# Performance work log

Hardware: AMD Instinct MI355X
Metric: run time of the kernel (lower is better)

Reference implementation:

```python
import jax, jax.numpy as jnp
import numpy as np

B, N, D_FEAT = 16, 1024, 64
NPOINT, RADIUS, NSAMPLE = 512, 0.2, 32
EPS = 1e-5


def _square_distance(src, dst):
    # src [b,S,3], dst [b,N,3] -> [b,S,N]
    d = -2.0 * jnp.einsum('bsc,bnc->bsn', src, dst)
    d = d + jnp.sum(src * src, -1)[:, :, None]
    d = d + jnp.sum(dst * dst, -1)[:, None, :]
    return d


def _fps(xyz, npoint):
    # xyz [b,N,3] -> indices [b,npoint]; seeded by point farthest from the mean
    b, n, _ = xyz.shape
    centroid = jnp.mean(xyz, axis=1, keepdims=True)
    distance = jnp.minimum(jnp.full((b, n), 1e10, xyz.dtype),
                           jnp.sum((xyz - centroid) ** 2, -1))
    farthest = jnp.argmax(distance, -1)
    bidx = jnp.arange(b)

    def body(carry, _):
        dist, far = carry
        c = xyz[bidx[:, None], far[:, None]]  # [b,1,3]
        dist = jnp.minimum(dist, jnp.sum((xyz - c) ** 2, -1))
        return (dist, jnp.argmax(dist, -1)), far

    _, idx = jax.lax.scan(body, (distance, farthest), None, length=npoint)
    return idx.T  # [b, npoint]


def _gather(points, idx):
    # points [b,N,C], idx [b,...] -> [b,...,C]
    return jax.vmap(lambda p, i: p[i])(points, idx)


def _query_ball(radius, nsample, xyz, new_xyz):
    # faithful to torch: mask out-of-radius with N, full sort, take first nsample,
    # replace sentinels by the first (closest-index) in-ball point
    b, n, _ = xyz.shape
    sqr = _square_distance(new_xyz, xyz)  # [b,S,N]
    idx = jnp.where(sqr > radius ** 2, n, jnp.arange(n)[None, None, :])
    idx = jnp.sort(idx, axis=-1)[:, :, :nsample]
    first = idx[:, :, :1]
    return jnp.where(idx == n, first, idx)


def _qbn(x):
    # QBN_RM training mode: divide by per-channel RMS of detached activations
    mean = jnp.mean(jax.lax.stop_gradient(x) ** 2, axis=(0, 2, 3))
    return x / jnp.sqrt(mean + EPS)[None, :, None, None]


def _qrelu(x):
    # scale each 3-vector by mod / max(mod, 1), coefficient detached
    b3, c, s, k = x.shape
    b = b3 // 3
    xd = jax.lax.stop_gradient(x).reshape(b, 3, c, s, k)
    mod = jnp.sqrt(jnp.sum(xd * xd, axis=1))  # [b,c,s,k]
    coeff = mod / jnp.maximum(mod, 1.0)
    return jnp.broadcast_to(coeff[:, None], (b, 3, c, s, k)).reshape(b3, c, s, k) * x


def _qmaxpool(x):
    # our_mpool1d with kernel (1, nsample): pick the max-modulus sample over K,
    # gather the same index for all 3 quaternion components
    b3, c, s, k = x.shape
    b = b3 // 3
    x5 = x.reshape(b, 3, c, s, k)
    mod = jnp.sum(jax.lax.stop_gradient(x5) ** 2, axis=1)  # argmax of mod == argmax of mod^2
    idx = jnp.argmax(mod, axis=-1)  # [b,c,s]
    idxb = jnp.broadcast_to(idx[:, None, :, :, None], (b, 3, c, s, 1))
    y = jnp.take_along_axis(x5, idxb, axis=-1)[..., 0]  # [b,3,c,s]
    return y.reshape(b3, c, s)


def setup_inputs() -> dict:
    key = jax.random.key(0)
    k1, k2, k3, k4, k5 = jax.random.split(key, 5)
    xyz = jax.random.normal(k1, (B, 3, N), dtype=jnp.float32)
    points = jax.random.normal(k2, (B * 3, D_FEAT, N), dtype=jnp.float32)
    W0 = jax.random.normal(k3, (64, 66), dtype=jnp.float32) * np.sqrt(2.0 / 66)
    W1 = jax.random.normal(k4, (64, 64), dtype=jnp.float32) * np.sqrt(2.0 / 64)
    W2 = jax.random.normal(k5, (128, 64), dtype=jnp.float32) * np.sqrt(2.0 / 64)
    return {"xyz": xyz, "points": points, "W0": W0, "W1": W1, "W2": W2}


def reference(xyz, points, W0, W1, W2):
    xyz_t = xyz.transpose(0, 2, 1)      # [B,N,3]
    pts_t = points.transpose(0, 2, 1)   # [B*3,N,D]

    fps_idx = _fps(xyz_t, NPOINT)                       # [B,S]
    new_xyz = _gather(xyz_t, fps_idx)                   # [B,S,3]
    idx = _query_ball(RADIUS, NSAMPLE, xyz_t, new_xyz)  # [B,S,K]

    g_xyz = _gather(xyz_t, idx)                         # [B,S,K,3]
    g_norm = g_xyz - new_xyz[:, :, None, :]
    gx = g_xyz.transpose(0, 3, 1, 2).reshape(B * 3, NPOINT, NSAMPLE, 1)
    gn = g_norm.transpose(0, 3, 1, 2).reshape(B * 3, NPOINT, NSAMPLE, 1)
    idx3 = jnp.broadcast_to(idx[:, None], (B, 3, NPOINT, NSAMPLE)).reshape(B * 3, NPOINT, NSAMPLE)
    gp = _gather(pts_t, idx3)                           # [B*3,S,K,D]

    x = jnp.concatenate([gn, gx, gp], axis=-1)          # [B*3,S,K,D+2]
    x = x.transpose(0, 3, 1, 2)                         # [B*3,D+2,S,K]
    for W in (W0, W1, W2):
        x = jnp.einsum('bcsk,oc->bosk', x, W)           # 1x1 conv, no bias
        x = _qrelu(_qbn(x))
    new_feat = _qmaxpool(x)                             # [B*3,128,S]
    return new_xyz.transpose(0, 2, 1), new_feat
```

## Files before the change

kernel.cpp:

```cpp
#include <hip/hip_runtime.h>

typedef unsigned int u32;
typedef unsigned long long u64;
typedef float v2f __attribute__((ext_vector_type(2)));

#define NB 16
#define NPT 1024
#define NP 512
#define NS 32
#define DF 64
#define RAD2 0.04f
#define EPSQ 1e-5f
#define CNTF 786432.0f
#define NGRP 8192
#define TCAP 96
#define TSLOT 128
#define NTILE_MAX 2731
#define NBALLBLK 4096
#define NFILLBLK 1366

__device__ __forceinline__ float rmul(float a, float b){ return __fmul_rn(a,b); }
__device__ __forceinline__ float radd(float a, float b){ return __fadd_rn(a,b); }
__device__ __forceinline__ float sq3(float a, float b, float c){
  return radd(radd(rmul(a,a), rmul(b,b)), rmul(c,c));
}

__device__ __forceinline__ float wave_sum64(float v){
  #pragma unroll
  for(int m=1;m<64;m<<=1) v += __shfl_xor(v, m, 64);
  return v;
}
__device__ __forceinline__ float half_sum32(float v){
  #pragma unroll
  for(int m=1;m<32;m<<=1) v += __shfl_xor(v, m, 64);
  return v;
}

#define DPPK(CTRL) do{ \
  unsigned _lo = (unsigned)k, _hi = (unsigned)(k>>32); \
  unsigned _mlo = (unsigned)__builtin_amdgcn_mov_dpp((int)_lo, (CTRL), 0xF, 0xF, true); \
  unsigned _mhi = (unsigned)__builtin_amdgcn_mov_dpp((int)_hi, (CTRL), 0xF, 0xF, true); \
  u64 _mk = ((u64)_mhi<<32) | _mlo; \
  k = (_mk > k) ? _mk : k; \
}while(0)

template<int PT>
__global__ __launch_bounds__(256) void fps_combo(const float* __restrict__ xyz,
                                                 float* __restrict__ out0,
                                                 const float* __restrict__ pts,
                                                 float* __restrict__ ptsT,
                                                 u32* __restrict__ witem,
                                                 int* __restrict__ idxb_full,
                                                 int* __restrict__ cnt_full,
                                                 int* __restrict__ farIdx){
#pragma clang fp contract(off)
  const int bid = blockIdx.x;
  const int t = threadIdx.x;

  if(bid >= 8){
    if(bid < 8 + NBALLBLK){
      const int row = (bid - 8)*4 + (t>>6);
      const int lane = t & 63;
      const int b = row >> 10;
      const int nc = row & 1023;
      const float* xb = xyz + b*3*NPT;
      const float s0 = xb[nc], s1 = xb[NPT+nc], s2 = xb[2*NPT+nc];
      const float ss = sq3(s0,s1,s2);
      int base = 0;
      int* rowp = idxb_full + row*NS;
      for(int chk=0; chk<16 && base<NS; ++chk){
        const int n = chk*64 + lane;
        float d0 = xb[n], d1 = xb[NPT+n], d2 = xb[2*NPT+n];
        float dd = sq3(d0,d1,d2);
        float p  = radd(radd(rmul(s0,d0), rmul(s1,d1)), rmul(s2,d2));
        float sqr = radd(radd(rmul(-2.0f,p), ss), dd);
        bool inc = !(sqr > RAD2);
        u64 mask = __ballot(inc);
        if(inc){
          int slot = base + __popcll(mask & ((1ull<<lane)-1ull));
          if(slot < NS) rowp[slot] = n;
        }
        base += __popcll(mask);
      }
      if(lane==0) cnt_full[row] = (base < NS) ? base : NS;
    } else {
      const int gid = (bid - 8 - NBALLBLK)*256 + t;
      if(gid < NTILE_MAX*TSLOT) witem[gid] = 0xFFFFFFFFu;
      if constexpr(PT){
        const int w = gid >> 6, ln = gid & 63;
        if(w < 48*16){
          const int b3 = w >> 4, n0 = (w & 15) << 6;
          const float* src = pts + (((size_t)b3*64 + ln) << 10);
          float* dst = ptsT + (((size_t)b3*1024 + n0) << 6) + ln;
          #pragma unroll 4
          for(int i=0;i<64;i++) dst[(size_t)i << 6] = src[n0 + i];
        }
      }
    }
    return;
  }

  __shared__ float4 plds[2048];
  if(t >= 64) return;
  __builtin_amdgcn_s_setprio(3);
  const int lane = t;
  const int half = lane >> 5;
  const int hl   = lane & 31;
  const int b    = 2*bid + half;
  const float* xb = xyz + b*3*NPT;

  v2f px2[16], py2[16], pz2[16], dist2[16];
  u32 loj[32];
  #pragma unroll
  for(int i=0;i<16;i++){
    const int n0 = 64*i + hl, n1 = n0 + 32;
    float x0v = xb[n0],        x1v = xb[n1];
    float y0v = xb[NPT+n0],    y1v = xb[NPT+n1];
    float z0v = xb[2*NPT+n0],  z1v = xb[2*NPT+n1];
    px2[i].x = x0v; px2[i].y = x1v;
    py2[i].x = y0v; py2[i].y = y1v;
    pz2[i].x = z0v; pz2[i].y = z1v;
    loj[2*i]   = 1023u - (u32)n0;
    loj[2*i+1] = 1023u - (u32)n1;
    plds[(half<<10) + n0] = make_float4(x0v, y0v, z0v, 0.f);
    plds[(half<<10) + n1] = make_float4(x1v, y1v, z1v, 0.f);
  }
  float sx=0.f, sy=0.f, sz=0.f;
  #pragma unroll
  for(int i=0;i<16;i++){
    sx += px2[i].x; sx += px2[i].y;
    sy += py2[i].x; sy += py2[i].y;
    sz += pz2[i].x; sz += pz2[i].y;
  }
  sx = half_sum32(sx); sy = half_sum32(sy); sz = half_sum32(sz);
  const float cx = sx/1024.f, cy = sy/1024.f, cz = sz/1024.f;
  {
    v2f cx2; cx2.x=cx; cx2.y=cx;
    v2f cy2; cy2.x=cy; cy2.y=cy;
    v2f cz2; cz2.x=cz; cz2.y=cz;
    #pragma unroll
    for(int i=0;i<16;i++){
      v2f dx = px2[i]-cx2, dy = py2[i]-cy2, dz = pz2[i]-cz2;
      v2f m1 = dx*dx, m2 = dy*dy, a1 = m1+m2, m3 = dz*dz, s2 = a1+m3;
      dist2[i].x = fminf(1e10f, s2.x);
      dist2[i].y = fminf(1e10f, s2.y);
    }
  }
  auto reduce2 = [&](int& fA, int& fB){
    u64 kk[16];
    #pragma unroll
    for(int i=0;i<16;i++){
      float a = dist2[i].x, bb = dist2[i].y;
      bool tk = bb > a;
      float dw = tk ? bb : a;
      u32   lw = tk ? loj[2*i+1] : loj[2*i];
      kk[i] = ((u64)__float_as_uint(dw)<<32) | lw;
    }
    #pragma unroll
    for(int i=0;i<8;i++){ u64 l=kk[2*i], r=kk[2*i+1]; kk[i] = (r>l)?r:l; }
    #pragma unroll
    for(int i=0;i<4;i++){ u64 l=kk[2*i], r=kk[2*i+1]; kk[i] = (r>l)?r:l; }
    #pragma unroll
    for(int i=0;i<2;i++){ u64 l=kk[2*i], r=kk[2*i+1]; kk[i] = (r>l)?r:l; }
    u64 k = (kk[1]>kk[0]) ? kk[1] : kk[0];
    DPPK(0xB1);
    DPPK(0x4E);
    DPPK(0x124);
    DPPK(0x128);
    DPPK(0x142);
    unsigned lo = (unsigned)k;
    fA = 1023 - __builtin_amdgcn_readlane((int)lo, 31);
    fB = 1023 - __builtin_amdgcn_readlane((int)lo, 63);
  };

  __asm__ volatile("s_waitcnt lgkmcnt(0)" ::: "memory");
  int farA, farB;
  reduce2(farA, farB);
  for(int it=0; it<NP; ++it){
    const int farv = (lane & 32) ? farB : farA;
    const float4 qv = plds[(half<<10) + farv];
    if(hl == 0){
      out0[(b*3+0)*NP + it] = qv.x;
      out0[(b*3+1)*NP + it] = qv.y;
      out0[(b*3+2)*NP + it] = qv.z;
      farIdx[b*NP + it] = farv;
    }
    v2f qx2; qx2.x=qv.x; qx2.y=qv.x;
    v2f qy2; qy2.x=qv.y; qy2.y=qv.y;
    v2f qz2; qz2.x=qv.z; qz2.y=qv.z;
    #pragma unroll
    for(int i=0;i<16;i++){
      v2f dx = px2[i]-qx2, dy = py2[i]-qy2, dz = pz2[i]-qz2;
      v2f m1 = dx*dx, m2 = dy*dy, a1 = m1+m2, m3 = dz*dz, s2 = a1+m3;
      dist2[i].x = fminf(dist2[i].x, s2.x);
      dist2[i].y = fminf(dist2[i].y, s2.y);
    }
    reduce2(farA, farB);
  }
}

__global__ __launch_bounds__(1024) void pack_kernel(const int* __restrict__ farIdx,
                                                    const int* __restrict__ cnt_full,
                                                    const int* __restrict__ idxb_full,
                                                    u32* __restrict__ witem,
                                                    int* __restrict__ ntile_dev,
                                                    int* __restrict__ cntb){
  const int t = threadIdx.x;
  const int lane = t & 63;
  const int wv = t >> 6;
  int c[8]; int rowid[8]; int s0 = 0;
  #pragma unroll
  for(int i=0;i<8;i++){
    const int g = t*8+i;
    const int far = farIdx[g];
    rowid[i] = ((g>>9)<<10) + far;
    c[i] = cnt_full[rowid[i]];
    cntb[g] = c[i];
    s0 += c[i];
  }
  int pre = s0;
  #pragma unroll
  for(int d=1; d<64; d<<=1){
    int v = __shfl_up(pre, d, 64);
    if(lane >= d) pre += v;
  }
  __shared__ int wsum[16];
  if(lane==63) wsum[wv] = pre;
  __syncthreads();
  int wo = 0;
  #pragma unroll
  for(int w=0;w<16;w++) if(w < wv) wo += wsum[w];
  int m = wo + pre - s0;
  if(t==1023) *ntile_dev = (wo + pre + TCAP - 1) / TCAP;
  #pragma unroll
  for(int i=0;i<8;i++){
    const int g = t*8+i; const int cc = c[i];
    const int tile = m / TCAP; const int slot = m - TCAP*tile;
    const int* rp = idxb_full + rowid[i]*NS;
    for(int j=0;j<cc;j++){
      witem[tile*TSLOT + slot + j] = (u32)((g<<15) | (j<<10) | rp[j]);
    }
    m += cc;
  }
}

template<int DEPTH, int PT>
__global__ __launch_bounds__(384) void pass_kernel(
  const float* __restrict__ xyz, const float* __restrict__ ptsrc,
  const float* __restrict__ W0, const float* __restrict__ W1, const float* __restrict__ W2,
  const float* __restrict__ out0, const u32* __restrict__ witem,
  const int* __restrict__ cntb, const int* __restrict__ ntile_dev,
  const float* __restrict__ inv1, const float* __restrict__ inv2,
  float* __restrict__ part, float* __restrict__ out1,
  int cache_tiles, float* __restrict__ cacheA, float* __restrict__ cacheB)
{
  const int t = threadIdx.x;
  const int c3 = t >> 7;
  const int r  = t & 127;
  const int lane = t & 63;
  const int wv = t >> 6;
  const int bi = blockIdx.x;

  if(bi >= *ntile_dev) return;
  const bool use_cache = (bi < cache_tiles);
  float* cslotA = cacheA + ((size_t)bi*TSLOT + r)*192 + (size_t)c3*64;
  float* cslotB = cacheB + ((size_t)bi*TSLOT + r)*192 + (size_t)c3*64;

  __shared__ float sq[3][128][17];
  __shared__ float wstat[6][128];
  for(int i=t; i<6*128; i+=384) (&wstat[0][0])[i] = 0.f;
  __syncthreads();

  const u32 w = witem[bi*TSLOT + r];
  const bool valid = (w != 0xFFFFFFFFu);
  const int bs = valid ? (int)(w >> 15) : 0;
  const int j  = valid ? (int)((w >> 10) & 31) : 1;
  const int n  = valid ? (int)(w & 1023) : 0;
  const int b = bs >> 9;
  const int s = bs & 511;
  const int b3 = b*3 + c3;
  const int cv = cntb[bs];
  const float wgt = valid ? ((j==0) ? (float)(33 - cv) : 1.0f) : 0.0f;

  float acc64[64];
  if(DEPTH >= 2 && use_cache){
    #pragma unroll
    for(int q=0;q<16;q++){
      float4 v = ((const float4*)cslotA)[q];
      acc64[4*q]=v.x; acc64[4*q+1]=v.y; acc64[4*q+2]=v.z; acc64[4*q+3]=v.w;
    }
  } else {
    const float gx = xyz[b3*NPT + n];
    const float cx = out0[b3*NP + s];
    float x0[66];
    x0[0] = gx - cx;
    x0[1] = gx;
    if constexpr(PT){
      const float4* pr4 = reinterpret_cast<const float4*>(ptsrc + (((size_t)b3<<10) + (size_t)n)*DF);
      #pragma unroll
      for(int q=0;q<16;q++){
        float4 v = pr4[q];
        x0[2+4*q] = v.x; x0[3+4*q] = v.y; x0[4+4*q] = v.z; x0[5+4*q] = v.w;
      }
    } else {
      const float* pr = ptsrc + ((size_t)b3*DF)*NPT + n;
      #pragma unroll
      for(int c=0;c<DF;c++) x0[2+c] = pr[(size_t)c*NPT];
    }
    #pragma unroll
    for(int ch=0; ch<4; ++ch){
      #pragma unroll
      for(int oo=0;oo<16;oo++){
        const int o = ch*16+oo;
        float a = 0.f;
        #pragma unroll
        for(int c=0;c<66;c++) a = fmaf(W0[o*66+c], x0[c], a);
        acc64[o] = a;
      }
    }
    if(DEPTH == 1 && use_cache){
      #pragma unroll
      for(int q=0;q<16;q++){
        float4 v; v.x=acc64[4*q]; v.y=acc64[4*q+1]; v.z=acc64[4*q+2]; v.w=acc64[4*q+3];
        ((float4*)cslotA)[q] = v;
      }
    }
  }

  if constexpr(DEPTH == 1){
    #pragma unroll
    for(int o=0;o<64;o++){
      float v = wave_sum64(acc64[o]*acc64[o]*wgt);
      if(lane==0) wstat[wv][o] += v;
    }
    __syncthreads();
    if(t < 64){
      float sv = 0.f;
      #pragma unroll
      for(int wq=0;wq<6;wq++) sv += wstat[wq][t];
      part[bi*64 + t] = sv;
    }
    return;
  }

  float y1[64];
  #pragma unroll
  for(int ch=0; ch<4; ++ch){
    float xp16[16];
    #pragma unroll
    for(int oo=0;oo<16;oo++){
      const int o = ch*16+oo;
      float xp = acc64[o] * inv1[o];
      xp16[oo] = xp;
      sq[c3][r][oo] = xp*xp;
    }
    __syncthreads();
    #pragma unroll
    for(int oo=0;oo<16;oo++){
      float m2 = (sq[0][r][oo] + sq[1][r][oo]) + sq[2][r][oo];
      float mod = sqrtf(m2);
      float cf = (mod >= 1.f) ? 1.f : mod;
      y1[ch*16+oo] = cf * xp16[oo];
    }
    __syncthreads();
  }

  float acc2[64];
  if(DEPTH == 3 && use_cache){
    #pragma unroll
    for(int q=0;q<16;q++){
      float4 v = ((const float4*)cslotB)[q];
      acc2[4*q]=v.x; acc2[4*q+1]=v.y; acc2[4*q+2]=v.z; acc2[4*q+3]=v.w;
    }
  } else {
    #pragma unroll
    for(int ch=0; ch<4; ++ch){
      #pragma unroll
      for(int oo=0;oo<16;oo++){
        const int o = ch*16+oo;
        float a = 0.f;
        #pragma unroll
        for(int c=0;c<64;c++) a = fmaf(W1[o*64+c], y1[c], a);
        acc2[o] = a;
      }
    }
    if(DEPTH == 2 && use_cache){
      #pragma unroll
      for(int q=0;q<16;q++){
        float4 v; v.x=acc2[4*q]; v.y=acc2[4*q+1]; v.z=acc2[4*q+2]; v.w=acc2[4*q+3];
        ((float4*)cslotB)[q] = v;
      }
    }
  }

  if constexpr(DEPTH == 2){
    #pragma unroll
    for(int o=0;o<64;o++){
      float v = wave_sum64(acc2[o]*acc2[o]*wgt);
      if(lane==0) wstat[wv][o] += v;
    }
    __syncthreads();
    if(t < 64){
      float sv = 0.f;
      #pragma unroll
      for(int wq=0;wq<6;wq++) sv += wstat[wq][t];
      part[bi*64 + t] = sv;
    }
    return;
  }

  float y2[64];
  #pragma unroll
  for(int ch=0; ch<4; ++ch){
    float xp16[16];
    #pragma unroll
    for(int oo=0;oo<16;oo++){
      const int o = ch*16+oo;
      float xp = acc2[o] * inv2[o];
      xp16[oo] = xp;
      sq[c3][r][oo] = xp*xp;
    }
    __syncthreads();
    #pragma unroll
    for(int oo=0;oo<16;oo++){
      float m2 = (sq[0][r][oo] + sq[1][r][oo]) + sq[2][r][oo];
      float mod = sqrtf(m2);
      float cf = (mod >= 1.f) ? 1.f : mod;
      y2[ch*16+oo] = cf * xp16[oo];
    }
    __syncthreads();
  }

  #pragma unroll
  for(int ch=0; ch<8; ++ch){
    float a3[16];
    #pragma unroll
    for(int oo=0;oo<16;oo++){
      const int o = ch*16+oo;
      float a = 0.f;
      #pragma unroll
      for(int c=0;c<64;c++) a = fmaf(W2[o*64+c], y2[c], a);
      a3[oo] = a;
      sq[c3][r][oo] = a;
    }
    __syncthreads();
    if(c3 == 0){
      #pragma unroll
      for(int oo=0;oo<16;oo++){
        float a0 = sq[0][r][oo], a1 = sq[1][r][oo], a2 = sq[2][r][oo];
        float m2 = radd(radd(rmul(a0,a0), rmul(a1,a1)), rmul(a2,a2));
        float v = wave_sum64(m2*wgt);
        if(lane==0) wstat[wv][ch*16+oo] += v;
        if(valid && j==0){
          float bvv = m2; int bjj = 0;
          for(int jj=1; jj<cv; ++jj){
            float c0 = sq[0][r+jj][oo], c1 = sq[1][r+jj][oo], c2 = sq[2][r+jj][oo];
            float mm = radd(radd(rmul(c0,c0), rmul(c1,c1)), rmul(c2,c2));
            if(mm > bvv){ bvv = mm; bjj = jj; }
          }
          const int o = ch*16+oo;
          #pragma unroll
          for(int cc=0;cc<3;cc++){
            out1[(((size_t)(3*b+cc))*128 + o)*NP + s] = sq[cc][r+bjj][oo];
          }
        }
      }
    }
    __syncthreads();
  }
  if(t < 128){
    part[bi*128 + t] = wstat[0][t] + wstat[1][t];
  }
}

__global__ __launch_bounds__(256) void fin_kernel(const float* __restrict__ part,
                                                  const int* __restrict__ ntile_dev, int nch,
                                                  float* __restrict__ inv){
  const int o = blockIdx.x;
  const int t = threadIdx.x;
  const int nblk = *ntile_dev;
  float sum = 0.f;
  for(int i=t; i<nblk; i+=256) sum += part[(size_t)i*nch + o];
  sum = wave_sum64(sum);
  __shared__ float red[4];
  if((t&63)==0) red[t>>6] = sum;
  __syncthreads();
  if(t==0){
    float tot = (red[0]+red[1])+(red[2]+red[3]);
    inv[o] = 1.0f / sqrtf(tot/CNTF + EPSQ);
  }
}

__global__ __launch_bounds__(256) void fin3_scale(const float* __restrict__ part3,
                                                  const int* __restrict__ ntile_dev,
                                                  float* __restrict__ out){
  const int o = blockIdx.x;
  const int t = threadIdx.x;
  const int nblk = *ntile_dev;
  float sum = 0.f;
  for(int i=t; i<nblk; i+=256) sum += part3[(size_t)i*128 + o];
  sum = wave_sum64(sum);
  __shared__ float red[4];
  __shared__ float sinv;
  if((t&63)==0) red[t>>6] = sum;
  __syncthreads();
  if(t==0){
    float tot = (red[0]+red[1])+(red[2]+red[3]);
    sinv = 1.0f / sqrtf(tot/CNTF + EPSQ);
  }
  __syncthreads();
  const float iv = sinv;
  float* base = out + NB*3*NP;
  const size_t str = (size_t)128*NP;
  for(int idx=t; idx<NB*NP; idx+=256){
    const int b = idx >> 9, s = idx & 511;
    size_t i0 = ((size_t)(b*3)*128 + o)*NP + s;
    float a0 = base[i0] * iv;
    float a1 = base[i0+str] * iv;
    float a2 = base[i0+2*str] * iv;
    float m2 = (a0*a0 + a1*a1) + a2*a2;
    float mod = sqrtf(m2);
    float cf = (mod >= 1.f) ? 1.f : mod;
    base[i0] = cf*a0; base[i0+str] = cf*a1; base[i0+2*str] = cf*a2;
  }
}

extern "C" void kernel_launch(void* const* d_in, const int* in_sizes, int n_in,
                              void* d_out, int out_size, void* d_ws, size_t ws_size,
                              hipStream_t stream){
  const float* xyz = (const float*)d_in[0];
  const float* pts = (const float*)d_in[1];
  const float* W0  = (const float*)d_in[2];
  const float* W1  = (const float*)d_in[3];
  const float* W2  = (const float*)d_in[4];
  float* out = (float*)d_out;

  char* p = (char*)d_ws;
  auto carve = [&](size_t bytes)->char*{
    char* q = p; p += (bytes + 255) & ~(size_t)255; return q;
  };
  int*   idxb_full = (int*)  carve((size_t)NB*NPT*NS*4);
  int*   cnt_full  = (int*)  carve((size_t)NB*NPT*4);
  int*   farIdx    = (int*)  carve((size_t)NGRP*4);
  int*   cntb      = (int*)  carve((size_t)NGRP*4);
  u32*   witem     = (u32*)  carve((size_t)NTILE_MAX*TSLOT*4);
  int*   ntile_dev = (int*)  carve(256);
  float* part1     = (float*)carve((size_t)NTILE_MAX*64*4);
  float* part2     = (float*)carve((size_t)NTILE_MAX*64*4);
  float* part3     = (float*)carve((size_t)NTILE_MAX*128*4);
  float* inv1      = (float*)carve(64*4);
  float* inv2      = (float*)carve(64*4);
  float* inv3      = (float*)carve(128*4);
  size_t base_need = (size_t)(p - (char*)d_ws);
  float* ptsT      = (float*)p;
  const size_t pt_bytes = (size_t)48*1024*64*4;
  const bool use_pt = (ws_size >= base_need + pt_bytes + (1u<<20));

  size_t fixed = base_need + (use_pt ? pt_bytes : 0);
  const size_t per_tile = (size_t)TSLOT*192*4*2;
  int cache_tiles = 0;
  if(ws_size > fixed + per_tile)
    cache_tiles = (int)(((ws_size - fixed) / per_tile));
  if(cache_tiles > NTILE_MAX) cache_tiles = NTILE_MAX;
  float* cacheA = (float*)((char*)d_ws + fixed);
  float* cacheB = cacheA + (size_t)cache_tiles*TSLOT*192;

  float* out1 = out + NB*3*NP;
  const int nblk = 8 + NBALLBLK + NFILLBLK;

  if(use_pt) fps_combo<1><<<nblk, 256, 0, stream>>>(xyz, out, pts, ptsT, witem, idxb_full, cnt_full, farIdx);
  else       fps_combo<0><<<nblk, 256, 0, stream>>>(xyz, out, pts, nullptr, witem, idxb_full, cnt_full, farIdx);

  pack_kernel<<<1, 1024, 0, stream>>>(farIdx, cnt_full, idxb_full, witem, ntile_dev, cntb);

  if(use_pt){
    pass_kernel<1,1><<<NTILE_MAX, 384, 0, stream>>>(xyz, ptsT, W0, W1, W2, out, witem, cntb, ntile_dev, nullptr, nullptr, part1, nullptr, cache_tiles, cacheA, cacheB);
    fin_kernel<<<64, 256, 0, stream>>>(part1, ntile_dev, 64, inv1);
    pass_kernel<2,1><<<NTILE_MAX, 384, 0, stream>>>(xyz, ptsT, W0, W1, W2, out, witem, cntb, ntile_dev, inv1, nullptr, part2, nullptr, cache_tiles, cacheA, cacheB);
    fin_kernel<<<64, 256, 0, stream>>>(part2, ntile_dev, 64, inv2);
    pass_kernel<3,1><<<NTILE_MAX, 384, 0, stream>>>(xyz, ptsT, W0, W1, W2, out, witem, cntb, ntile_dev, inv1, inv2, part3, out1, cache_tiles, cacheA, cacheB);
  } else {
    pass_kernel<1,0><<<NTILE_MAX, 384, 0, stream>>>(xyz, pts, W0, W1, W2, out, witem, cntb, ntile_dev, nullptr, nullptr, part1, nullptr, cache_tiles, cacheA, cacheB);
    fin_kernel<<<64, 256, 0, stream>>>(part1, ntile_dev, 64, inv1);
    pass_kernel<2,0><<<NTILE_MAX, 384, 0, stream>>>(xyz, pts, W0, W1, W2, out, witem, cntb, ntile_dev, inv1, nullptr, part2, nullptr, cache_tiles, cacheA, cacheB);
    fin_kernel<<<64, 256, 0, stream>>>(part2, ntile_dev, 64, inv2);
    pass_kernel<3,0><<<NTILE_MAX, 384, 0, stream>>>(xyz, pts, W0, W1, W2, out, witem, cntb, ntile_dev, inv1, inv2, part3, out1, cache_tiles, cacheA, cacheB);
  }
  fin3_scale<<<128, 256, 0, stream>>>(part3, ntile_dev, out);
}
```

Before: 749.3 us.

## Fuse BN stat finalisation into pass kernels and use persistent grid

Removes the two separate fin_kernel launches: each pass block now recomputes the per-channel inverse RMS from the partial sums of the previous pass into shared memory. Pass kernels switch to a fixed grid of 512 persistent blocks that loop over tiles. DEPTH 3 with cached tiles now skips recomputing layer 0 and layer 1 entirely and reads the cached layer-1 output directly. This saves launch overhead and redundant work, at the cost of every block redundantly reducing all partials and less parallelism per tile.

```diff
diff --git a/kernel.cpp b/kernel.cpp
--- a/kernel.cpp
+++ b/kernel.cpp
@@ -18,6 +18,7 @@
 #define NTILE_MAX 2731
 #define NBALLBLK 4096
 #define NFILLBLK 1366
+#define NPGRID 512
 
 __device__ __forceinline__ float rmul(float a, float b){ return __fmul_rn(a,b); }
 __device__ __forceinline__ float radd(float a, float b){ return __fadd_rn(a,b); }
@@ -163,11 +164,7 @@
     #pragma unroll
     for(int i=0;i<2;i++){ u64 l=kk[2*i], r=kk[2*i+1]; kk[i] = (r>l)?r:l; }
     u64 k = (kk[1]>kk[0]) ? kk[1] : kk[0];
-    DPPK(0xB1);
-    DPPK(0x4E);
-    DPPK(0x124);
-    DPPK(0x128);
-    DPPK(0x142);
+    DPPK(0xB1); DPPK(0x4E); DPPK(0x124); DPPK(0x128); DPPK(0x142);
     unsigned lo = (unsigned)k;
     fA = 1023 - __builtin_amdgcn_readlane((int)lo, 31);
     fB = 1023 - __builtin_amdgcn_readlane((int)lo, 63);
@@ -244,13 +241,41 @@
   }
 }
 
+__device__ __forceinline__ void compute_inv(const float* __restrict__ part, int ntile, int nch,
+                                            float* invsh, float (*redb)[8], int t, int lane){
+  for(int o0=0; o0<nch; o0+=8){
+    float s[8];
+    #pragma unroll
+    for(int k2=0;k2<8;k2++) s[k2]=0.f;
+    if(t < 256){
+      for(int i=t; i<ntile; i+=256){
+        const float* pp = part + (size_t)i*nch + o0;
+        #pragma unroll
+        for(int k2=0;k2<8;k2++) s[k2] += pp[k2];
+      }
+    }
+    #pragma unroll
+    for(int k2=0;k2<8;k2++) s[k2] = wave_sum64(s[k2]);
+    if(t < 256 && lane==0){
+      #pragma unroll
+      for(int k2=0;k2<8;k2++) redb[t>>6][k2] = s[k2];
+    }
+    __syncthreads();
+    if(t < 8){
+      float tot = (redb[0][t]+redb[1][t])+(redb[2][t]+redb[3][t]);
+      invsh[o0+t] = 1.0f/sqrtf(tot/CNTF + EPSQ);
+    }
+    __syncthreads();
+  }
+}
+
 template<int DEPTH, int PT>
 __global__ __launch_bounds__(384) void pass_kernel(
   const float* __restrict__ xyz, const float* __restrict__ ptsrc,
   const float* __restrict__ W0, const float* __restrict__ W1, const float* __restrict__ W2,
   const float* __restrict__ out0, const u32* __restrict__ witem,
   const int* __restrict__ cntb, const int* __restrict__ ntile_dev,
-  const float* __restrict__ inv1, const float* __restrict__ inv2,
+  const float* __restrict__ part_in1, const float* __restrict__ part_in2,
   float* __restrict__ part, float* __restrict__ out1,
   int cache_tiles, float* __restrict__ cacheA, float* __restrict__ cacheB)
 {
@@ -259,235 +284,232 @@
   const int r  = t & 127;
   const int lane = t & 63;
   const int wv = t >> 6;
-  const int bi = blockIdx.x;
-
-  if(bi >= *ntile_dev) return;
-  const bool use_cache = (bi < cache_tiles);
-  float* cslotA = cacheA + ((size_t)bi*TSLOT + r)*192 + (size_t)c3*64;
-  float* cslotB = cacheB + ((size_t)bi*TSLOT + r)*192 + (size_t)c3*64;
+
+  const int ntile = *ntile_dev;
+  if(blockIdx.x >= ntile) return;
 
   __shared__ float sq[3][128][17];
   __shared__ float wstat[6][128];
-  for(int i=t; i<6*128; i+=384) (&wstat[0][0])[i] = 0.f;
-  __syncthreads();
-
-  const u32 w = witem[bi*TSLOT + r];
-  const bool valid = (w != 0xFFFFFFFFu);
-  const int bs = valid ? (int)(w >> 15) : 0;
-  const int j  = valid ? (int)((w >> 10) & 31) : 1;
-  const int n  = valid ? (int)(w & 1023) : 0;
-  const int b = bs >> 9;
-  const int s = bs & 511;
-  const int b3 = b*3 + c3;
-  const int cv = cntb[bs];
-  const float wgt = valid ? ((j==0) ? (float)(33 - cv) : 1.0f) : 0.0f;
-
-  float acc64[64];
-  if(DEPTH >= 2 && use_cache){
-    #pragma unroll
-    for(int q=0;q<16;q++){
-      float4 v = ((const float4*)cslotA)[q];
-      acc64[4*q]=v.x; acc64[4*q+1]=v.y; acc64[4*q+2]=v.z; acc64[4*q+3]=v.w;
-    }
-  } else {
-    const float gx = xyz[b3*NPT + n];
-    const float cx = out0[b3*NP + s];
-    float x0[66];
-    x0[0] = gx - cx;
-    x0[1] = gx;
-    if constexpr(PT){
-      const float4* pr4 = reinterpret_cast<const float4*>(ptsrc + (((size_t)b3<<10) + (size_t)n)*DF);
+  __shared__ float invsh1[64];
+  __shared__ float invsh2[64];
+  __shared__ float redb[4][8];
+
+  if constexpr(DEPTH >= 2) compute_inv(part_in1, ntile, 64, invsh1, redb, t, lane);
+  if constexpr(DEPTH == 3) compute_inv(part_in2, ntile, 64, invsh2, redb, t, lane);
+
+  for(int bi = blockIdx.x; bi < ntile; bi += NPGRID){
+    const bool use_cache = (bi < cache_tiles);
+    float* cslotA = cacheA + ((size_t)bi*TSLOT + r)*192 + (size_t)c3*64;
+    float* cslotB = cacheB + ((size_t)bi*TSLOT + r)*192 + (size_t)c3*64;
+
+    for(int i=t; i<6*128; i+=384) (&wstat[0][0])[i] = 0.f;
+    __syncthreads();
+
+    const u32 w = witem[bi*TSLOT + r];
+    const bool valid = (w != 0xFFFFFFFFu);
+    const int bs = valid ? (int)(w >> 15) : 0;
+    const int j  = valid ? (int)((w >> 10) & 31) : 1;
+    const int n  = valid ? (int)(w & 1023) : 0;
+    const int b = bs >> 9;
+    const int s = bs & 511;
+    const int b3 = b*3 + c3;
+    const int cv = cntb[bs];
+    const float wgt = valid ? ((j==0) ? (float)(33 - cv) : 1.0f) : 0.0f;
+
+    float acc2[64];
+    bool skip01 = (DEPTH == 3) && use_cache;
+
+    if(!skip01){
+      float acc64[64];
+      if(DEPTH >= 2 && use_cache){
+        #pragma unroll
+        for(int q=0;q<16;q++){
+          float4 v = ((const float4*)cslotA)[q];
+          acc64[4*q]=v.x; acc64[4*q+1]=v.y; acc64[4*q+2]=v.z; acc64[4*q+3]=v.w;
+        }
+      } else {
+        const float gx = xyz[b3*NPT + n];
+        const float cx = out0[b3*NP + s];
+        float x0[66];
+        x0[0] = gx - cx;
+        x0[1] = gx;
+        if constexpr(PT){
+          const float4* pr4 = reinterpret_cast<const float4*>(ptsrc + (((size_t)b3<<10) + (size_t)n)*DF);
+          #pragma unroll
+          for(int q=0;q<16;q++){
+            float4 v = pr4[q];
+            x0[2+4*q] = v.x; x0[3+4*q] = v.y; x0[4+4*q] = v.z; x0[5+4*q] = v.w;
+          }
+        } else {
+          const float* pr = ptsrc + ((size_t)b3*DF)*NPT + n;
+          #pragma unroll
+          for(int c=0;c<DF;c++) x0[2+c] = pr[(size_t)c*NPT];
+        }
+        #pragma unroll
+        for(int ch=0; ch<4; ++ch){
+          #pragma unroll
+          for(int oo=0;oo<16;oo++){
+            const int o = ch*16+oo;
+            float a = 0.f;
+            #pragma unroll
+            for(int c=0;c<66;c++) a = fmaf(W0[o*66+c], x0[c], a);
+            acc64[o] = a;
+          }
+        }
+        if(DEPTH == 1 && use_cache){
+          #pragma unroll
+          for(int q=0;q<16;q++){
+            float4 v; v.x=acc64[4*q]; v.y=acc64[4*q+1]; v.z=acc64[4*q+2]; v.w=acc64[4*q+3];
+            ((float4*)cslotA)[q] = v;
+          }
+        }
+      }
+
+      if constexpr(DEPTH == 1){
+        #pragma unroll
+        for(int o=0;o<64;o++){
+          float v = wave_sum64(acc64[o]*acc64[o]*wgt);
+          if(lane==0) wstat[wv][o] += v;
+        }
+        __syncthreads();
+        if(t < 64){
+          float sv = 0.f;
+          #pragma unroll
+          for(int wq=0;wq<6;wq++) sv += wstat[wq][t];
+          part[bi*64 + t] = sv;
+        }
+        __syncthreads();
+        continue;
+      }
+
+      float y1[64];
+      #pragma unroll
+      for(int ch=0; ch<4; ++ch){
+        float xp16[16];
+        #pragma unroll
+        for(int oo=0;oo<16;oo++){
+          const int o = ch*16+oo;
+          float xp = acc64[o] * invsh1[o];
+          xp16[oo] = xp;
+          sq[c3][r][oo] = xp*xp;
+        }
+        __syncthreads();
+        #pragma unroll
+        for(int oo=0;oo<16;oo++){
+          float m2 = (sq[0][r][oo] + sq[1][r][oo]) + sq[2][r][oo];
+          float mod = sqrtf(m2);
+          float cf = (mod >= 1.f) ? 1.f : mod;
+          y1[ch*16+oo] = cf * xp16[oo];
+        }
+        __syncthreads();
+      }
+
+      #pragma unroll
+      for(int ch=0; ch<4; ++ch){
+        #pragma unroll
+        for(int oo=0;oo<16;oo++){
+          const int o = ch*16+oo;
+          float a = 0.f;
+          #pragma unroll
+          for(int c=0;c<64;c++) a = fmaf(W1[o*64+c], y1[c], a);
+          acc2[o] = a;
+        }
+      }
+      if(DEPTH == 2 && use_cache){
+        #pragma unroll
+        for(int q=0;q<16;q++){
+          float4 v; v.x=acc2[4*q]; v.y=acc2[4*q+1]; v.z=acc2[4*q+2]; v.w=acc2[4*q+3];
+          ((float4*)cslotB)[q] = v;
+        }
+      }
+    } else {
       #pragma unroll
       for(int q=0;q<16;q++){
-        float4 v = pr4[q];
-        x0[2+4*q] = v.x; x0[3+4*q] = v.y; x0[4+4*q] = v.z; x0[5+4*q] = v.w;
-      }
-    } else {
-      const float* pr = ptsrc + ((size_t)b3*DF)*NPT + n;
+        float4 v = ((const float4*)cslotB)[q];
+        acc2[4*q]=v.x; acc2[4*q+1]=v.y; acc2[4*q+2]=v.z; acc2[4*q+3]=v.w;
+      }
+    }
+
+    if constexpr(DEPTH == 2){
       #pragma unroll
-      for(int c=0;c<DF;c++) x0[2+c] = pr[(size_t)c*NPT];
-    }
-    #pragma unroll
-    for(int ch=0; ch<4; ++ch){
+      for(int o=0;o<64;o++){
+        float v = wave_sum64(acc2[o]*acc2[o]*wgt);
+        if(lane==0) wstat[wv][o] += v;
+      }
+      __syncthreads();
+      if(t < 64){
+        float sv = 0.f;
+        #pragma unroll
+        for(int wq=0;wq<6;wq++) sv += wstat[wq][t];
+        part[bi*64 + t] = sv;
+      }
+      __syncthreads();
+      continue;
+    }
+
+    if constexpr(DEPTH == 3){
+      float y2[64];
       #pragma unroll
-      for(int oo=0;oo<16;oo++){
-        const int o = ch*16+oo;
-        float a = 0.f;
-        #pragma unroll
-        for(int c=0;c<66;c++) a = fmaf(W0[o*66+c], x0[c], a);
-        acc64[o] = a;
-      }
-    }
-    if(DEPTH == 1 && use_cache){
+      for(int ch=0; ch<4; ++ch){
+        float xp16[16];
+        #pragma unroll
+        for(int oo=0;oo<16;oo++){
+          const int o = ch*16+oo;
+          float xp = acc2[o] * invsh2[o];
+          xp16[oo] = xp;
+          sq[c3][r][oo] = xp*xp;
+        }
+        __syncthreads();
+        #pragma unroll
+        for(int oo=0;oo<16;oo++){
+          float m2 = (sq[0][r][oo] + sq[1][r][oo]) + sq[2][r][oo];
+          float mod = sqrtf(m2);
+          float cf = (mod >= 1.f) ? 1.f : mod;
+          y2[ch*16+oo] = cf * xp16[oo];
+        }
+        __syncthreads();
+      }
+
       #pragma unroll
-      for(int q=0;q<16;q++){
-        float4 v; v.x=acc64[4*q]; v.y=acc64[4*q+1]; v.z=acc64[4*q+2]; v.w=acc64[4*q+3];
-        ((float4*)cslotA)[q] = v;
-      }
-    }
-  }
-
-  if constexpr(DEPTH == 1){
-    #pragma unroll
-    for(int o=0;o<64;o++){
-      float v = wave_sum64(acc64[o]*acc64[o]*wgt);
-      if(lane==0) wstat[wv][o] += v;
-    }
-    __syncthreads();
-    if(t < 64){
-      float sv = 0.f;
-      #pragma unroll
-      for(int wq=0;wq<6;wq++) sv += wstat[wq][t];
-      part[bi*64 + t] = sv;
-    }
-    return;
-  }
-
-  float y1[64];
-  #pragma unroll
-  for(int ch=0; ch<4; ++ch){
-    float xp16[16];
-    #pragma unroll
-    for(int oo=0;oo<16;oo++){
-      const int o = ch*16+oo;
-      float xp = acc64[o] * inv1[o];
-      xp16[oo] = xp;
-      sq[c3][r][oo] = xp*xp;
-    }
-    __syncthreads();
-    #pragma unroll
-    for(int oo=0;oo<16;oo++){
-      float m2 = (sq[0][r][oo] + sq[1][r][oo]) + sq[2][r][oo];
-      float mod = sqrtf(m2);
-      float cf = (mod >= 1.f) ? 1.f : mod;
-      y1[ch*16+oo] = cf * xp16[oo];
-    }
-    __syncthreads();
-  }
-
-  float acc2[64];
-  if(DEPTH == 3 && use_cache){
-    #pragma unroll
-    for(int q=0;q<16;q++){
-      float4 v = ((const float4*)cslotB)[q];
-      acc2[4*q]=v.x; acc2[4*q+1]=v.y; acc2[4*q+2]=v.z; acc2[4*q+3]=v.w;
-    }
-  } else {
-    #pragma unroll
-    for(int ch=0; ch<4; ++ch){
-      #pragma unroll
-      for(int oo=0;oo<16;oo++){
-        const int o = ch*16+oo;
-        float a = 0.f;
-        #pragma unroll
-        for(int c=0;c<64;c++) a = fmaf(W1[o*64+c], y1[c], a);
-        acc2[o] = a;
-      }
-    }
-    if(DEPTH == 2 && use_cache){
-      #pragma unroll
-      for(int q=0;q<16;q++){
-        float4 v; v.x=acc2[4*q]; v.y=acc2[4*q+1]; v.z=acc2[4*q+2]; v.w=acc2[4*q+3];
-        ((float4*)cslotB)[q] = v;
-      }
-    }
-  }
-
-  if constexpr(DEPTH == 2){
-    #pragma unroll
-    for(int o=0;o<64;o++){
-      float v = wave_sum64(acc2[o]*acc2[o]*wgt);
-      if(lane==0) wstat[wv][o] += v;
-    }
-    __syncthreads();
-    if(t < 64){
-      float sv = 0.f;
-      #pragma unroll
-      for(int wq=0;wq<6;wq++) sv += wstat[wq][t];
-      part[bi*64 + t] = sv;
-    }
-    return;
-  }
-
-  float y2[64];
-  #pragma unroll
-  for(int ch=0; ch<4; ++ch){
-    float xp16[16];
-    #pragma unroll
-    for(int oo=0;oo<16;oo++){
-      const int o = ch*16+oo;
-      float xp = acc2[o] * inv2[o];
-      xp16[oo] = xp;
-      sq[c3][r][oo] = xp*xp;
-    }
-    __syncthreads();
-    #pragma unroll
-    for(int oo=0;oo<16;oo++){
-      float m2 = (sq[0][r][oo] + sq[1][r][oo]) + sq[2][r][oo];
-      float mod = sqrtf(m2);
-      float cf = (mod >= 1.f) ? 1.f : mod;
-      y2[ch*16+oo] = cf * xp16[oo];
-    }
-    __syncthreads();
-  }
-
-  #pragma unroll
-  for(int ch=0; ch<8; ++ch){
-    float a3[16];
-    #pragma unroll
-    for(int oo=0;oo<16;oo++){
-      const int o = ch*16+oo;
-      float a = 0.f;
-      #pragma unroll
-      for(int c=0;c<64;c++) a = fmaf(W2[o*64+c], y2[c], a);
-      a3[oo] = a;
-      sq[c3][r][oo] = a;
-    }
-    __syncthreads();
-    if(c3 == 0){
-      #pragma unroll
-      for(int oo=0;oo<16;oo++){
-        float a0 = sq[0][r][oo], a1 = sq[1][r][oo], a2 = sq[2][r][oo];
-        float m2 = radd(radd(rmul(a0,a0), rmul(a1,a1)), rmul(a2,a2));
-        float v = wave_sum64(m2*wgt);
-        if(lane==0) wstat[wv][ch*16+oo] += v;
-        if(valid && j==0){
-          float bvv = m2; int bjj = 0;
-          for(int jj=1; jj<cv; ++jj){
-            float c0 = sq[0][r+jj][oo], c1 = sq[1][r+jj][oo], c2 = sq[2][r+jj][oo];
-            float mm = radd(radd(rmul(c0,c0), rmul(c1,c1)), rmul(c2,c2));
-            if(mm > bvv){ bvv = mm; bjj = jj; }
+      for(int ch=0; ch<8; ++ch){
+        #pragma unroll
+        for(int oo=0;oo<16;oo++){
+          const int o = ch*16+oo;
+          float a = 0.f;
+          #pragma unroll
+          for(int c=0;c<64;c++) a = fmaf(W2[o*64+c], y2[c], a);
+          sq[c3][r][oo] = a;
+        }
+        __syncthreads();
+        if(c3 == 0){
+          #pragma unroll
+          for(int oo=0;oo<16;oo++){
+            float a0 = sq[0][r][oo], a1 = sq[1][r][oo], a2 = sq[2][r][oo];
+            float m2 = radd(radd(rmul(a0,a0), rmul(a1,a1)), rmul(a2,a2));
+            float v = wave_sum64(m2*wgt);
+            if(lane==0) wstat[wv][ch*16+oo] += v;
+            if(valid && j==0){
+              float bvv = m2; int bjj = 0;
+              for(int jj=1; jj<cv; ++jj){
+                float c0 = sq[0][r+jj][oo], c1 = sq[1][r+jj][oo], c2 = sq[2][r+jj][oo];
+                float mm = radd(radd(rmul(c0,c0), rmul(c1,c1)), rmul(c2,c2));
+                if(mm > bvv){ bvv = mm; bjj = jj; }
+              }
+              const int o = ch*16+oo;
+              #pragma unroll
+              for(int cc=0;cc<3;cc++){
+                out1[(((size_t)(3*b+cc))*128 + o)*NP + s] = sq[cc][r+bjj][oo];
+              }
+            }
           }
-          const int o = ch*16+oo;
-          #pragma unroll
-          for(int cc=0;cc<3;cc++){
-            out1[(((size_t)(3*b+cc))*128 + o)*NP + s] = sq[cc][r+bjj][oo];
-          }
-        }
-      }
-    }
-    __syncthreads();
-  }
-  if(t < 128){
-    part[bi*128 + t] = wstat[0][t] + wstat[1][t];
-  }
-}
-
-__global__ __launch_bounds__(256) void fin_kernel(const float* __restrict__ part,
-                                                  const int* __restrict__ ntile_dev, int nch,
-                                                  float* __restrict__ inv){
-  const int o = blockIdx.x;
-  const int t = threadIdx.x;
-  const int nblk = *ntile_dev;
-  float sum = 0.f;
-  for(int i=t; i<nblk; i+=256) sum += part[(size_t)i*nch + o];
-  sum = wave_sum64(sum);
-  __shared__ float red[4];
-  if((t&63)==0) red[t>>6] = sum;
-  __syncthreads();
-  if(t==0){
-    float tot = (red[0]+red[1])+(red[2]+red[3]);
-    inv[o] = 1.0f / sqrtf(tot/CNTF + EPSQ);
+        }
+        __syncthreads();
+      }
+      if(t < 128){
+        part[bi*128 + t] = wstat[0][t] + wstat[1][t];
+      }
+      __syncthreads();
+    }
   }
 }
 
@@ -548,9 +570,6 @@
   float* part1     = (float*)carve((size_t)NTILE_MAX*64*4);
   float* part2     = (float*)carve((size_t)NTILE_MAX*64*4);
   float* part3     = (float*)carve((size_t)NTILE_MAX*128*4);
-  float* inv1      = (float*)carve(64*4);
-  float* inv2      = (float*)carve(64*4);
-  float* inv3      = (float*)carve(128*4);
   size_t base_need = (size_t)(p - (char*)d_ws);
   float* ptsT      = (float*)p;
   const size_t pt_bytes = (size_t)48*1024*64*4;
@@ -560,7 +579,7 @@
   const size_t per_tile = (size_t)TSLOT*192*4*2;
   int cache_tiles = 0;
   if(ws_size > fixed + per_tile)
-    cache_tiles = (int)(((ws_size - fixed) / per_tile));
+    cache_tiles = (int)((ws_size - fixed) / per_tile);
   if(cache_tiles > NTILE_MAX) cache_tiles = NTILE_MAX;
   float* cacheA = (float*)((char*)d_ws + fixed);
   float* cacheB = cacheA + (size_t)cache_tiles*TSLOT*192;
@@ -574,17 +593,13 @@
   pack_kernel<<<1, 1024, 0, stream>>>(farIdx, cnt_full, idxb_full, witem, ntile_dev, cntb);
 
   if(use_pt){
-    pass_kernel<1,1><<<NTILE_MAX, 384, 0, stream>>>(xyz, ptsT, W0, W1, W2, out, witem, cntb, ntile_dev, nullptr, nullptr, part1, nullptr, cache_tiles, cacheA, cacheB);
-    fin_kernel<<<64, 256, 0, stream>>>(part1, ntile_dev, 64, inv1);
-    pass_kernel<2,1><<<NTILE_MAX, 384, 0, stream>>>(xyz, ptsT, W0, W1, W2, out, witem, cntb, ntile_dev, inv1, nullptr, part2, nullptr, cache_tiles, cacheA, cacheB);
-    fin_kernel<<<64, 256, 0, stream>>>(part2, ntile_dev, 64, inv2);
-    pass_kernel<3,1><<<NTILE_MAX, 384, 0, stream>>>(xyz, ptsT, W0, W1, W2, out, witem, cntb, ntile_dev, inv1, inv2, part3, out1, cache_tiles, cacheA, cacheB);
+    pass_kernel<1,1><<<NPGRID, 384, 0, stream>>>(xyz, ptsT, W0, W1, W2, out, witem, cntb, ntile_dev, nullptr, nullptr, part1, nullptr, cache_tiles, cacheA, cacheB);
+    pass_kernel<2,1><<<NPGRID, 384, 0, stream>>>(xyz, ptsT, W0, W1, W2, out, witem, cntb, ntile_dev, part1, nullptr, part2, nullptr, cache_tiles, cacheA, cacheB);
+    pass_kernel<3,1><<<NPGRID, 384, 0, stream>>>(xyz, ptsT, W0, W1, W2, out, witem, cntb, ntile_dev, part1, part2, part3, out1, cache_tiles, cacheA, cacheB);
   } else {
-    pass_kernel<1,0><<<NTILE_MAX, 384, 0, stream>>>(xyz, pts, W0, W1, W2, out, witem, cntb, ntile_dev, nullptr, nullptr, part1, nullptr, cache_tiles, cacheA, cacheB);
-    fin_kernel<<<64, 256, 0, stream>>>(part1, ntile_dev, 64, inv1);
-    pass_kernel<2,0><<<NTILE_MAX, 384, 0, stream>>>(xyz, pts, W0, W1, W2, out, witem, cntb, ntile_dev, inv1, nullptr, part2, nullptr, cache_tiles, cacheA, cacheB);
-    fin_kernel<<<64, 256, 0, stream>>>(part2, ntile_dev, 64, inv2);
-    pass_kernel<3,0><<<NTILE_MAX, 384, 0, stream>>>(xyz, pts, W0, W1, W2, out, witem, cntb, ntile_dev, inv1, inv2, part3, out1, cache_tiles, cacheA, cacheB);
+    pass_kernel<1,0><<<NPGRID, 384, 0, stream>>>(xyz, pts, W0, W1, W2, out, witem, cntb, ntile_dev, nullptr, nullptr, part1, nullptr, cache_tiles, cacheA, cacheB);
+    pass_kernel<2,0><<<NPGRID, 384, 0, stream>>>(xyz, pts, W0, W1, W2, out, witem, cntb, ntile_dev, part1, nullptr, part2, nullptr, cache_tiles, cacheA, cacheB);
+    pass_kernel<3,0><<<NPGRID, 384, 0, stream>>>(xyz, pts, W0, W1, W2, out, witem, cntb, ntile_dev, part1, part2, part3, out1, cache_tiles, cacheA, cacheB);
   }
   fin3_scale<<<128, 256, 0, stream>>>(part3, ntile_dev, out);
 }
```

Measured after the change: 918.4 us. 22.6% more time.
